# Optimization experiments

Measured on AMD Instinct MI355X. Metric: run time of the kernel, lower is better.

The kernel has to match this reference:

```python
import jax, jax.numpy as jnp
import numpy as np

H = 1024
NUM_HEADS = 16
E = 4
I = H * 4 // E  # expert intermediate size = 1024
EPS = 1e-6


def layer_norm(x, g, b):
    mu = jnp.mean(x, axis=-1, keepdims=True)
    var = jnp.mean(jnp.square(x - mu), axis=-1, keepdims=True)
    return (x - mu) * jax.lax.rsqrt(var + EPS) * g + b


def setup_inputs() -> dict:
    key = jax.random.key(0)
    ks = jax.random.split(key, 12)
    B, Nq, Nkv = 4, 1024, 2048
    inp = {
        "query": jax.random.normal(ks[0], (B, Nq, H), jnp.float32),
        "key_value": jax.random.normal(ks[1], (B, Nkv, H), jnp.float32),
        "Wq": jax.random.normal(ks[2], (H, H), jnp.float32) * 0.02,
        "bq": jnp.zeros((H,), jnp.float32),
        "Wk": jax.random.normal(ks[3], (H, H), jnp.float32) * 0.02,
        "bk": jnp.zeros((H,), jnp.float32),
        "Wv": jax.random.normal(ks[4], (H, H), jnp.float32) * 0.02,
        "bv": jnp.zeros((H,), jnp.float32),
        "Wo": jax.random.normal(ks[5], (H, H), jnp.float32) * 0.02,
        "bo": jnp.zeros((H,), jnp.float32),
        "g1": jnp.ones((H,), jnp.float32),
        "b1": jnp.zeros((H,), jnp.float32),
        "g2": jnp.ones((H,), jnp.float32),
        "b2": jnp.zeros((H,), jnp.float32),
        "gate_up": jax.random.normal(ks[6], (E, H, 2 * I), jnp.float32) * 0.02,
        "down": jax.random.normal(ks[7], (E, I, H), jnp.float32) * 0.02,
    }
    return inp


def reference(query, key_value, Wq, bq, Wk, bk, Wv, bv, Wo, bo,
              g1, b1, g2, b2, gate_up, down):
    B, Nq, _ = query.shape
    Nkv = key_value.shape[1]
    d = H // NUM_HEADS
    scale = d ** -0.5

    # ---- cross-attention with pre-norm + residual ----
    x = layer_norm(query, g1, b1)
    q = (x @ Wq + bq).reshape(B, Nq, NUM_HEADS, d)
    k = (key_value @ Wk + bk).reshape(B, Nkv, NUM_HEADS, d)
    v = (key_value @ Wv + bv).reshape(B, Nkv, NUM_HEADS, d)
    scores = jnp.einsum("bqhd,bkhd->bhqk", q, k) * scale
    attn = jax.nn.softmax(scores, axis=-1)
    ctx = jnp.einsum("bhqk,bkhd->bqhd", attn, v).reshape(B, Nq, H)
    x = query + (ctx @ Wo + bo)

    # ---- token-routed MoE SwiGLU MLP (expert = pos % E) ----
    residual = x
    h = layer_norm(x, g2, b2)
    outs = []
    for e in range(E):
        xe = h[:, e::E]                      # [B, Nq/E, H] tokens routed to expert e
        gu = xe @ gate_up[e]                 # [B, Nq/E, 2I]
        gate, up = gu[..., :I], gu[..., I:]
        inter = jax.nn.silu(gate) * up
        outs.append(inter @ down[e])         # [B, Nq/E, H]
    moe = jnp.stack(outs, axis=2).reshape(B, Nq, H)  # interleave back to position order
    return residual + moe
```

## Files before the change

### kernel.cpp

```cpp
#include <hip/hip_runtime.h>
#include <hip/hip_bf16.h>

typedef unsigned short u16;
typedef float f32x4 __attribute__((ext_vector_type(4)));
typedef short s16x8 __attribute__((ext_vector_type(8)));

__device__ __forceinline__ u16 f2b(float f) {
    union { float f; unsigned u; } c; c.f = f;
    unsigned r = c.u + 0x7fffu + ((c.u >> 16) & 1u);
    return (u16)(r >> 16);
}
__device__ __forceinline__ unsigned pkbf16(float a, float b) {
    union { __hip_bfloat162 h; unsigned u; } c;
    c.h = __float22bfloat162_rn(float2{a, b});
    return c.u;
}

#define ASYNC_COPY16(gp, lp)                                                       \
    __builtin_amdgcn_global_load_lds(                                              \
        (const __attribute__((address_space(1))) void*)(gp),                       \
        (__attribute__((address_space(3))) void*)(lp), 16, 0, 0)

__device__ __forceinline__ void transcast_body(const float* __restrict__ Wz,
                                               u16* __restrict__ Wtz,
                                               int K, int N, int bx, int by,
                                               int permute) {
    __shared__ float tile[64][65];
    const int n0 = bx * 64, k0 = by * 64;
    const int tid = threadIdx.x;
    const int tx = tid & 15, ty = tid >> 4;
#pragma unroll
    for (int it = 0; it < 4; it++) {
        int r = ty + it * 16;
        float4 v = *(const float4*)&Wz[(size_t)(k0 + r) * N + n0 + tx * 4];
        tile[r][tx * 4 + 0] = v.x;
        tile[r][tx * 4 + 1] = v.y;
        tile[r][tx * 4 + 2] = v.z;
        tile[r][tx * 4 + 3] = v.w;
    }
    __syncthreads();
    int n = tid >> 2;
    int ks = (tid & 3) * 16;
    int drow = n0 + n;
    if (permute) drow = (drow < 1024) ? 2 * drow : 2 * (drow - 1024) + 1;
    u16* dst = &Wtz[(size_t)drow * K + k0 + ks];
#pragma unroll
    for (int h = 0; h < 2; h++) {
        uint4 o;
        o.x = pkbf16(tile[ks + h * 8 + 0][n], tile[ks + h * 8 + 1][n]);
        o.y = pkbf16(tile[ks + h * 8 + 2][n], tile[ks + h * 8 + 3][n]);
        o.z = pkbf16(tile[ks + h * 8 + 4][n], tile[ks + h * 8 + 5][n]);
        o.w = pkbf16(tile[ks + h * 8 + 6][n], tile[ks + h * 8 + 7][n]);
        *(uint4*)(dst + h * 8) = o;
    }
}

__device__ __forceinline__ void cast_body(const float* __restrict__ x,
                                          u16* __restrict__ y, int blk) {
    int id = blk * 256 + threadIdx.x;
    const float* p = x + (size_t)id * 8;
    float4 a = *(const float4*)p;
    float4 b = *(const float4*)(p + 4);
    uint4 o;
    o.x = pkbf16(a.x, a.y);
    o.y = pkbf16(a.z, a.w);
    o.z = pkbf16(b.x, b.y);
    o.w = pkbf16(b.z, b.w);
    *(uint4*)(y + (size_t)id * 8) = o;
}

__device__ __forceinline__ void ln_body(const float* __restrict__ x,
                                        const float* __restrict__ g,
                                        const float* __restrict__ bb,
                                        u16* __restrict__ out, int token, int pack) {
    int tid = threadIdx.x;
    const float* row = x + (size_t)token * 1024;
    float4 v = *(const float4*)(row + tid * 4);
    float s1 = v.x + v.y + v.z + v.w;
    float s2 = v.x * v.x + v.y * v.y + v.z * v.z + v.w * v.w;
#pragma unroll
    for (int off = 32; off > 0; off >>= 1) {
        s1 += __shfl_down(s1, off);
        s2 += __shfl_down(s2, off);
    }
    __shared__ float ws1[4], ws2[4];
    int wave = tid >> 6;
    if ((tid & 63) == 0) { ws1[wave] = s1; ws2[wave] = s2; }
    __syncthreads();
    float t1 = ws1[0] + ws1[1] + ws1[2] + ws1[3];
    float t2 = ws2[0] + ws2[1] + ws2[2] + ws2[3];
    float mean = t1 * (1.f / 1024.f);
    float var = t2 * (1.f / 1024.f) - mean * mean;
    float rstd = rsqrtf(var + 1e-6f);
    size_t dest = token;
    if (pack) {
        int bq = token >> 10, q = token & 1023;
        dest = (size_t)(q & 3) * 1024 + (size_t)bq * 256 + (q >> 2);
    }
    int c = tid * 4;
    float4 gv = *(const float4*)(g + c);
    float4 bv = *(const float4*)(bb + c);
    uint2 o;
    o.x = pkbf16((v.x - mean) * rstd * gv.x + bv.x, (v.y - mean) * rstd * gv.y + bv.y);
    o.y = pkbf16((v.z - mean) * rstd * gv.z + bv.z, (v.w - mean) * rstd * gv.w + bv.w);
    *(uint2*)&out[dest * 1024 + c] = o;
}

__global__ __launch_bounds__(256) void ln_kernel(const float* __restrict__ x,
                                                 const float* __restrict__ g,
                                                 const float* __restrict__ bb,
                                                 u16* __restrict__ out, int pack) {
    ln_body(x, g, bb, out, blockIdx.x, pack);
}

__global__ __launch_bounds__(256) void prep_kernel(
    const float* __restrict__ Wq, const float* __restrict__ Wk,
    const float* __restrict__ Wv, const float* __restrict__ Wo,
    u16* __restrict__ wqt, u16* __restrict__ wkt,
    u16* __restrict__ wvt, u16* __restrict__ wot,
    const float* __restrict__ gate_up, u16* __restrict__ gut,
    const float* __restrict__ down, u16* __restrict__ dnt,
    const float* __restrict__ key_value, u16* __restrict__ kvbf,
    const float* __restrict__ query, const float* __restrict__ g1,
    const float* __restrict__ b1, u16* __restrict__ xn) {
    const int idx = blockIdx.x;
    if (idx < 1024) {
        int z = idx >> 8, r = idx & 255;
        const float* W = (z == 0) ? Wq : (z == 1) ? Wk : (z == 2) ? Wv : Wo;
        u16* O = (z == 0) ? wqt : (z == 1) ? wkt : (z == 2) ? wvt : wot;
        transcast_body(W, O, 1024, 1024, r >> 4, r & 15, 0);
    } else if (idx < 3072) {
        int t = idx - 1024, z = t >> 9, r = t & 511;
        transcast_body(gate_up + (size_t)z * 2097152, gut + (size_t)z * 2097152,
                       1024, 2048, r >> 4, r & 15, 1);
    } else if (idx < 4096) {
        int t = idx - 3072, z = t >> 8, r = t & 255;
        transcast_body(down + (size_t)z * 1048576, dnt + (size_t)z * 1048576,
                       1024, 1024, r >> 4, r & 15, 0);
    } else if (idx < 8192) {
        cast_body(key_value, kvbf, idx - 4096);
    } else {
        ln_body(query, g1, b1, xn, idx - 8192, 0);
    }
}

template <int BM>
__device__ __forceinline__ void gemm_body(
    u16* As, u16* Bs,
    const u16* __restrict__ Ab, const u16* __restrict__ Bb,
    const float* __restrict__ bias0, const float* __restrict__ bias1, int biasSplit,
    const float* __restrict__ resid,
    float* __restrict__ outF, u16* __restrict__ outH, u16* __restrict__ outH2,
    int N, int K, long long oStride, int z, int mode, float outScale,
    int m0, int n0) {
    constexpr int NJ = (BM == 128) ? 4 : 2;
    const int tid = threadIdx.x;
    const int wave = tid >> 6, lane = tid & 63;
    const int wm = (BM == 128) ? (wave >> 1) * 64 : 0;
    const int wn = (BM == 128) ? (wave & 1) * 64 : wave * 32;
    const int quad = lane >> 4, l16 = lane & 15;
    f32x4 acc[4][NJ] = {};
    for (int k0 = 0; k0 < K; k0 += 64) {
#pragma unroll
        for (int i = 0; i < BM / 32; i++) {
            int id = tid + i * 256;
            int row = id >> 3, c = id & 7;
            int srcseg = c ^ (row & 7);
            ASYNC_COPY16(&Ab[(size_t)(m0 + row) * K + k0 + srcseg * 8],
                         As + (size_t)(wave * 64 + i * 256) * 8);
        }
#pragma unroll
        for (int i = 0; i < 4; i++) {
            int id = tid + i * 256;
            int row = id >> 3, c = id & 7;
            int srcseg = c ^ (row & 7);
            ASYNC_COPY16(&Bb[(size_t)(n0 + row) * K + k0 + srcseg * 8],
                         Bs + (size_t)(wave * 64 + i * 256) * 8);
        }
        __syncthreads();
#pragma unroll
        for (int kk = 0; kk < 2; kk++) {
            s16x8 af[4], bfr[NJ];
#pragma unroll
            for (int i = 0; i < 4; i++) {
                int row = wm + i * 16 + l16;
                af[i] = *(const s16x8*)&As[row * 64 + ((kk * 4 + quad) ^ (row & 7)) * 8];
            }
#pragma unroll
            for (int j = 0; j < NJ; j++) {
                int row = wn + j * 16 + l16;
                bfr[j] = *(const s16x8*)&Bs[row * 64 + ((kk * 4 + quad) ^ (row & 7)) * 8];
            }
#pragma unroll
            for (int i = 0; i < 4; i++)
#pragma unroll
                for (int j = 0; j < NJ; j++)
                    acc[i][j] = __builtin_amdgcn_mfma_f32_16x16x32_bf16(af[i], bfr[j], acc[i][j], 0, 0, 0);
        }
        __syncthreads();
    }
#pragma unroll
    for (int i = 0; i < 4; i++) {
#pragma unroll
        for (int j = 0; j < NJ; j++) {
            int col = n0 + wn + j * 16 + l16;
            float bv = 0.f;
            if (bias0) bv = (col < biasSplit) ? bias0[col] : bias1[col - biasSplit];
            if (mode == 3) {
                float vr[4];
#pragma unroll
                for (int r = 0; r < 4; r++) vr[r] = acc[i][j][r] + bv;
                int row0 = m0 + wm + i * 16 + quad * 4;
                if (col < 1024) {
#pragma unroll
                    for (int r = 0; r < 4; r++)
                        outH[(size_t)(row0 + r) * 1024 + col] = f2b(vr[r]);
                } else {
                    int bb2 = row0 >> 11, key = row0 & 2047;
                    int hh = (col - 1024) >> 6, d = (col - 1024) & 63;
                    uint2 dw;
                    dw.x = pkbf16(vr[0], vr[1]);
                    dw.y = pkbf16(vr[2], vr[3]);
                    *(uint2*)&outH2[(((size_t)bb2 * 16 + hh) * 64 + d) * 2048 + key] = dw;
                }
                continue;
            }
#pragma unroll
            for (int r = 0; r < 4; r++) {
                int row = m0 + wm + i * 16 + quad * 4 + r;
                float v = acc[i][j][r] + bv;
                if (mode == 2) {
                    float other = __shfl_xor(v, 1);
                    if (!(lane & 1)) {
                        float res = (v / (1.f + __expf(-v))) * other;
                        outH[(size_t)z * oStride + (size_t)row * (N >> 1) + (col >> 1)] = f2b(res);
                    }
                } else if (mode == 1) {
                    int bb2 = row >> 8, qi = row & 255;
                    size_t oidx = ((size_t)bb2 * 1024 + (size_t)z + 4 * (size_t)qi) * N + col;
                    outF[oidx] = v + resid[oidx];
                } else {
                    size_t oidx = (size_t)z * oStride + (size_t)row * N + col;
                    if (resid) v += resid[oidx];
                    if (outF) outF[oidx] = v;
                    else outH[oidx] = f2b(v * outScale);
                }
            }
        }
    }
}

template <int BM>
__global__ __launch_bounds__(256) void gemm_t(
    const u16* __restrict__ A, const u16* __restrict__ Bt,
    const float* __restrict__ bias0, const float* __restrict__ bias1, int biasSplit,
    const float* __restrict__ resid,
    float* __restrict__ outF, u16* __restrict__ outH, u16* __restrict__ outH2,
    int N, int K,
    long long aStride, long long bStride, long long oStride,
    int mode, float outScale) {
    extern __shared__ __align__(16) u16 ldsb[];
    const int z = blockIdx.z;
    gemm_body<BM>(ldsb, ldsb + BM * 64,
                  A + (size_t)z * aStride, Bt + (size_t)z * bStride,
                  bias0, bias1, biasSplit, resid, outF, outH, outH2,
                  N, K, oStride, z, mode, outScale,
                  blockIdx.y * BM, blockIdx.x * 128);
}

__global__ __launch_bounds__(256) void gemm_qkv(
    const u16* __restrict__ xn, const u16* __restrict__ wqt,
    const float* __restrict__ bq,
    const u16* __restrict__ kvbf, const u16* __restrict__ kvw,
    const float* __restrict__ bk, const float* __restrict__ bv,
    u16* __restrict__ qb, u16* __restrict__ kvb, u16* __restrict__ vtb,
    float qscale) {
    extern __shared__ __align__(16) u16 ldsb[];
    const int bid = blockIdx.x;
    if (bid < 1024) {
        gemm_body<128>(ldsb, ldsb + 128 * 64, kvbf, kvw,
                       bk, bv, 1024, nullptr, nullptr, kvb, vtb,
                       2048, 1024, 0, 0, 3, 1.f,
                       (bid >> 4) * 128, (bid & 15) * 128);
    } else {
        int t = bid - 1024;
        gemm_body<64>(ldsb, ldsb + 64 * 64, xn, wqt,
                      bq, bq, 1 << 30, nullptr, nullptr, qb, nullptr,
                      1024, 1024, 0, 0, 0, qscale,
                      (t >> 3) * 64, (t & 7) * 128);
    }
}

__global__ __launch_bounds__(256) void flash_attn(
    const u16* __restrict__ Q, const u16* __restrict__ Kb,
    const u16* __restrict__ VT, u16* __restrict__ O) {
    const int lidx = blockIdx.x;
    const int xcd = lidx & 7, slot = lidx >> 3;
    const int g = xcd + 8 * (slot >> 4);
    const int qt = slot & 15;
    const int b = g >> 4, h = g & 15;
    const int tid = threadIdx.x, wave = tid >> 6, lane = tid & 63;
    const int quad = lane >> 4, l16 = lane & 15;
    const int q0 = qt * 64 + wave * 16;

    __shared__ __align__(16) u16 Ks[64 * 64];
    __shared__ __align__(16) u16 Vs[64 * 64];

    const size_t qrow = ((size_t)b * 1024 + q0 + l16) * 1024 + (size_t)h * 64;
    s16x8 qf0 = *(const s16x8*)&Q[qrow + quad * 8];
    s16x8 qf1 = *(const s16x8*)&Q[qrow + 32 + quad * 8];

    f32x4 o[4] = {};
    float l = 0.f;

    const u16* Kbh = Kb + ((size_t)b * 2048) * 1024 + (size_t)h * 64;
    const u16* VTbh = VT + (((size_t)b * 16 + h) * 64) * 2048;
    const uint4* Ks128 = (const uint4*)Ks;
    const uint4* Vs128 = (const uint4*)Vs;

    const int srow = tid >> 3, sc = tid & 7;
    const int ga = 4 * (sc >> 2) + 2 * (sc & 1);
    const int o8 = ((sc >> 1) & 1) * 8;

    for (int kc = 0; kc < 2048; kc += 64) {
        __syncthreads();
#pragma unroll
        for (int i = 0; i < 2; i++) {
            int id = tid + i * 256;
            int row = id >> 3;
            int srcseg = (id & 7) ^ (row & 7);
            ASYNC_COPY16(Kbh + (size_t)(kc + row) * 1024 + srcseg * 8,
                         &Ks[(size_t)(wave * 64 + i * 256) * 8]);
        }
#pragma unroll
        for (int i = 0; i < 2; i++) {
            int row = srow + i * 32;
            uint4 v = *(const uint4*)(VTbh + (size_t)row * 2048 + kc + sc * 8);
            char* rowp = (char*)&Vs[row * 64];
            *(uint2*)(rowp + ((ga ^ (row & 7)) * 16) + o8) = uint2{v.x, v.y};
            *(uint2*)(rowp + (((ga + 1) ^ (row & 7)) * 16) + o8) = uint2{v.z, v.w};
        }
        __syncthreads();

        f32x4 s[4];
#pragma unroll
        for (int kt = 0; kt < 4; kt++) {
            int row = kt * 16 + l16;
            union { uint4 v; s16x8 f; } a0, a1;
            a0.v = Ks128[row * 8 + (quad ^ (row & 7))];
            a1.v = Ks128[row * 8 + ((4 + quad) ^ (row & 7))];
            f32x4 acc = {};
            acc = __builtin_amdgcn_mfma_f32_16x16x32_bf16(a0.f, qf0, acc, 0, 0, 0);
            acc = __builtin_amdgcn_mfma_f32_16x16x32_bf16(a1.f, qf1, acc, 0, 0, 0);
            s[kt] = acc;
        }

        float p[16], rs = 0.f;
#pragma unroll
        for (int kt = 0; kt < 4; kt++)
#pragma unroll
            for (int r = 0; r < 4; r++) {
                float e = exp2f(s[kt][r]);
                p[kt * 4 + r] = e;
                rs += e;
            }
        rs += __shfl_xor(rs, 16);
        rs += __shfl_xor(rs, 32);
        l += rs;

        uint2 dw[4];
#pragma unroll
        for (int kt = 0; kt < 4; kt++) {
            dw[kt].x = pkbf16(p[kt * 4 + 0], p[kt * 4 + 1]);
            dw[kt].y = pkbf16(p[kt * 4 + 2], p[kt * 4 + 3]);
        }

#pragma unroll
        for (int c2 = 0; c2 < 2; c2++) {
            union { uint4 v; s16x8 f; } pf;
            pf.v = uint4{dw[2 * c2].x, dw[2 * c2].y, dw[2 * c2 + 1].x, dw[2 * c2 + 1].y};
#pragma unroll
            for (int dt = 0; dt < 4; dt++) {
                int row = dt * 16 + l16;
                union { uint4 v; s16x8 f; } vf;
                vf.v = Vs128[row * 8 + ((c2 * 4 + quad) ^ (row & 7))];
                o[dt] = __builtin_amdgcn_mfma_f32_16x16x32_bf16(vf.f, pf.f, o[dt], 0, 0, 0);
            }
        }
    }

    float inv = 1.f / l;
    size_t orow = ((size_t)b * 1024 + q0 + l16) * 1024 + (size_t)h * 64;
#pragma unroll
    for (int dt = 0; dt < 4; dt++) {
        uint2 dw;
        dw.x = pkbf16(o[dt][0] * inv, o[dt][1] * inv);
        dw.y = pkbf16(o[dt][2] * inv, o[dt][3] * inv);
        *(uint2*)&O[orow + dt * 16 + quad * 4] = dw;
    }
}

extern "C" void kernel_launch(void* const* d_in, const int* in_sizes, int n_in,
                              void* d_out, int out_size, void* d_ws, size_t ws_size,
                              hipStream_t stream) {
    (void)in_sizes; (void)n_in; (void)out_size; (void)ws_size;
    const float* query     = (const float*)d_in[0];
    const float* key_value = (const float*)d_in[1];
    const float* Wq = (const float*)d_in[2];
    const float* bq = (const float*)d_in[3];
    const float* Wk = (const float*)d_in[4];
    const float* bk = (const float*)d_in[5];
    const float* Wv = (const float*)d_in[6];
    const float* bv = (const float*)d_in[7];
    const float* Wo = (const float*)d_in[8];
    const float* bo = (const float*)d_in[9];
    const float* g1 = (const float*)d_in[10];
    const float* b1 = (const float*)d_in[11];
    const float* g2 = (const float*)d_in[12];
    const float* b2 = (const float*)d_in[13];
    const float* gate_up = (const float*)d_in[14];
    const float* down    = (const float*)d_in[15];
    float* out = (float*)d_out;

    char* wsb = (char*)d_ws;
    size_t off = 0;
    auto alloc = [&](size_t bytes) {
        char* p = wsb + off;
        off += (bytes + 255) & ~(size_t)255;
        return (void*)p;
    };
    u16* buf8a = (u16*)alloc((size_t)4096 * 1024 * 2);
    u16* qb    = (u16*)alloc((size_t)4096 * 1024 * 2);
    u16* kvb   = (u16*)alloc((size_t)8192 * 1024 * 2);
    u16* vtb   = (u16*)alloc((size_t)8192 * 1024 * 2);
    u16* kvbf  = (u16*)alloc((size_t)8192 * 1024 * 2);
    float* x2  = (float*)alloc((size_t)4096 * 1024 * 4);
    u16* wqt   = (u16*)alloc((size_t)1024 * 1024 * 2);
    u16* kvw   = (u16*)alloc((size_t)2048 * 1024 * 2);
    u16* wot   = (u16*)alloc((size_t)1024 * 1024 * 2);
    u16* gut   = (u16*)alloc((size_t)4 * 2048 * 1024 * 2);
    u16* dnt   = (u16*)alloc((size_t)4 * 1024 * 1024 * 2);
    u16* xn = buf8a; u16* ctx = buf8a; u16* hp = buf8a;
    u16* inter = kvbf;
    const int BIG = 1 << 30;
    const float QSCALE = 0.125f * 1.44269504f;

    prep_kernel<<<12288, 256, 0, stream>>>(
        Wq, Wk, Wv, Wo, wqt, kvw, kvw + (size_t)1024 * 1024, wot,
        gate_up, gut, down, dnt, key_value, kvbf, query, g1, b1, xn);
    gemm_qkv<<<1536, 256, 32768, stream>>>(xn, wqt, bq, kvbf, kvw, bk, bv,
                                           qb, kvb, vtb, QSCALE);
    flash_attn<<<1024, 256, 0, stream>>>(qb, kvb, vtb, ctx);
    gemm_t<64><<<dim3(8, 64, 1), 256, 24576, stream>>>(ctx, wot, bo, bo, BIG,
        query, x2, nullptr, nullptr, 1024, 1024, 0, 0, 0, 0, 1.f);
    ln_kernel<<<4096, 256, 0, stream>>>(x2, g2, b2, hp, 1);
    gemm_t<64><<<dim3(16, 16, 4), 256, 24576, stream>>>(hp, gut, nullptr, nullptr, BIG,
        nullptr, nullptr, inter, nullptr, 2048, 1024,
        (long long)1024 * 1024, (long long)2048 * 1024, (long long)1024 * 1024, 2, 1.f);
    gemm_t<64><<<dim3(8, 16, 4), 256, 24576, stream>>>(inter, dnt, nullptr, nullptr, BIG,
        x2, out, nullptr, nullptr, 1024, 1024,
        (long long)1024 * 1024, (long long)1024 * 1024, 0, 1, 1.f);
}
```

Measured before the change: 390.8 us.

## Double-buffer flash attention, pre-swizzle V tiles, process 32 queries per wave

The QKV GEMM now writes V^T in a per-64-key chunk layout that already carries the LDS swizzle, so flash attention can stage V with async global-to-LDS copies instead of register loads plus scattered LDS stores. K/V tiles are double-buffered, so the next chunk loads while the current one computes, leaving one barrier per iteration. Each wave now handles two 16-row query blocks, which reuses every K/V fragment read for twice the MFMAs, and the grid is halved. The row-sum shuffles are deferred to the end. The cost is more registers per thread and double the LDS per block, which may reduce occupancy.

New measurement: 392.7 us. Within noise of the previous version (+0.5%).

```diff
diff --git a/kernel.cpp b/kernel.cpp
--- a/kernel.cpp
+++ b/kernel.cpp
@@ -218,10 +218,15 @@
                 } else {
                     int bb2 = row0 >> 11, key = row0 & 2047;
                     int hh = (col - 1024) >> 6, d = (col - 1024) & 63;
+                    int cc = key >> 6, kk = key & 63;
+                    int kk4 = kk >> 4, q4 = (kk >> 2) & 3;
+                    int seg = (((kk4 >> 1) << 2) | q4) ^ (d & 7);
+                    int half = kk4 & 1;
                     uint2 dw;
                     dw.x = pkbf16(vr[0], vr[1]);
                     dw.y = pkbf16(vr[2], vr[3]);
-                    *(uint2*)&outH2[(((size_t)bb2 * 16 + hh) * 64 + d) * 2048 + key] = dw;
+                    *(uint2*)&outH2[((((size_t)bb2 * 16 + hh) * 32 + cc) * 64 + d) * 64
+                                    + seg * 8 + half * 4] = dw;
                 }
                 continue;
             }
@@ -296,107 +301,120 @@
     const u16* __restrict__ VT, u16* __restrict__ O) {
     const int lidx = blockIdx.x;
     const int xcd = lidx & 7, slot = lidx >> 3;
-    const int g = xcd + 8 * (slot >> 4);
-    const int qt = slot & 15;
+    const int g = xcd + 8 * (slot >> 3);
+    const int qt = slot & 7;
     const int b = g >> 4, h = g & 15;
     const int tid = threadIdx.x, wave = tid >> 6, lane = tid & 63;
     const int quad = lane >> 4, l16 = lane & 15;
-    const int q0 = qt * 64 + wave * 16;
-
-    __shared__ __align__(16) u16 Ks[64 * 64];
-    __shared__ __align__(16) u16 Vs[64 * 64];
-
-    const size_t qrow = ((size_t)b * 1024 + q0 + l16) * 1024 + (size_t)h * 64;
-    s16x8 qf0 = *(const s16x8*)&Q[qrow + quad * 8];
-    s16x8 qf1 = *(const s16x8*)&Q[qrow + 32 + quad * 8];
-
-    f32x4 o[4] = {};
-    float l = 0.f;
+    const int q0 = qt * 128 + wave * 32;
+
+    __shared__ __align__(16) u16 Ks[2][64 * 64];
+    __shared__ __align__(16) u16 Vs[2][64 * 64];
+
+    const size_t qrowA = ((size_t)b * 1024 + q0 + l16) * 1024 + (size_t)h * 64;
+    const size_t qrowB = qrowA + (size_t)16 * 1024;
+    s16x8 qA0 = *(const s16x8*)&Q[qrowA + quad * 8];
+    s16x8 qA1 = *(const s16x8*)&Q[qrowA + 32 + quad * 8];
+    s16x8 qB0 = *(const s16x8*)&Q[qrowB + quad * 8];
+    s16x8 qB1 = *(const s16x8*)&Q[qrowB + 32 + quad * 8];
+
+    f32x4 oA[4] = {}, oB[4] = {};
+    float lA = 0.f, lB = 0.f;
 
     const u16* Kbh = Kb + ((size_t)b * 2048) * 1024 + (size_t)h * 64;
-    const u16* VTbh = VT + (((size_t)b * 16 + h) * 64) * 2048;
-    const uint4* Ks128 = (const uint4*)Ks;
-    const uint4* Vs128 = (const uint4*)Vs;
-
-    const int srow = tid >> 3, sc = tid & 7;
-    const int ga = 4 * (sc >> 2) + 2 * (sc & 1);
-    const int o8 = ((sc >> 1) & 1) * 8;
-
-    for (int kc = 0; kc < 2048; kc += 64) {
-        __syncthreads();
+    const u16* Vbh = VT + ((size_t)(b * 16 + h) * 32) * 4096;
+
+    auto stage = [&](int c, int buf) {
+        const int kc = c * 64;
+        u16* Kd = &Ks[buf][0];
+        u16* Vd = &Vs[buf][0];
 #pragma unroll
         for (int i = 0; i < 2; i++) {
             int id = tid + i * 256;
             int row = id >> 3;
             int srcseg = (id & 7) ^ (row & 7);
             ASYNC_COPY16(Kbh + (size_t)(kc + row) * 1024 + srcseg * 8,
-                         &Ks[(size_t)(wave * 64 + i * 256) * 8]);
-        }
+                         Kd + (size_t)(wave * 64 + i * 256) * 8);
+        }
+        const u16* Vc = Vbh + (size_t)c * 4096;
 #pragma unroll
         for (int i = 0; i < 2; i++) {
-            int row = srow + i * 32;
-            uint4 v = *(const uint4*)(VTbh + (size_t)row * 2048 + kc + sc * 8);
-            char* rowp = (char*)&Vs[row * 64];
-            *(uint2*)(rowp + ((ga ^ (row & 7)) * 16) + o8) = uint2{v.x, v.y};
-            *(uint2*)(rowp + (((ga + 1) ^ (row & 7)) * 16) + o8) = uint2{v.z, v.w};
-        }
+            ASYNC_COPY16(Vc + (size_t)(tid + i * 256) * 8,
+                         Vd + (size_t)(wave * 64 + i * 256) * 8);
+        }
+    };
+
+    stage(0, 0);
+    for (int c = 0; c < 32; c++) {
         __syncthreads();
-
-        f32x4 s[4];
+        if (c < 31) stage(c + 1, (c + 1) & 1);
+        const uint4* Kp = (const uint4*)&Ks[c & 1][0];
+        const uint4* Vp = (const uint4*)&Vs[c & 1][0];
+
+        f32x4 sA[4], sB[4];
 #pragma unroll
         for (int kt = 0; kt < 4; kt++) {
             int row = kt * 16 + l16;
             union { uint4 v; s16x8 f; } a0, a1;
-            a0.v = Ks128[row * 8 + (quad ^ (row & 7))];
-            a1.v = Ks128[row * 8 + ((4 + quad) ^ (row & 7))];
+            a0.v = Kp[row * 8 + (quad ^ (row & 7))];
+            a1.v = Kp[row * 8 + ((4 + quad) ^ (row & 7))];
             f32x4 acc = {};
-            acc = __builtin_amdgcn_mfma_f32_16x16x32_bf16(a0.f, qf0, acc, 0, 0, 0);
-            acc = __builtin_amdgcn_mfma_f32_16x16x32_bf16(a1.f, qf1, acc, 0, 0, 0);
-            s[kt] = acc;
-        }
-
-        float p[16], rs = 0.f;
-#pragma unroll
-        for (int kt = 0; kt < 4; kt++)
-#pragma unroll
-            for (int r = 0; r < 4; r++) {
-                float e = exp2f(s[kt][r]);
-                p[kt * 4 + r] = e;
-                rs += e;
-            }
-        rs += __shfl_xor(rs, 16);
-        rs += __shfl_xor(rs, 32);
-        l += rs;
-
-        uint2 dw[4];
+            acc = __builtin_amdgcn_mfma_f32_16x16x32_bf16(a0.f, qA0, acc, 0, 0, 0);
+            sA[kt] = __builtin_amdgcn_mfma_f32_16x16x32_bf16(a1.f, qA1, acc, 0, 0, 0);
+            f32x4 accB = {};
+            accB = __builtin_amdgcn_mfma_f32_16x16x32_bf16(a0.f, qB0, accB, 0, 0, 0);
+            sB[kt] = __builtin_amdgcn_mfma_f32_16x16x32_bf16(a1.f, qB1, accB, 0, 0, 0);
+        }
+
+        uint2 dwA[4], dwB[4];
+        float rsA = 0.f, rsB = 0.f;
 #pragma unroll
         for (int kt = 0; kt < 4; kt++) {
-            dw[kt].x = pkbf16(p[kt * 4 + 0], p[kt * 4 + 1]);
-            dw[kt].y = pkbf16(p[kt * 4 + 2], p[kt * 4 + 3]);
-        }
+            float p0 = exp2f(sA[kt][0]), p1 = exp2f(sA[kt][1]);
+            float p2 = exp2f(sA[kt][2]), p3 = exp2f(sA[kt][3]);
+            rsA += (p0 + p1) + (p2 + p3);
+            dwA[kt].x = pkbf16(p0, p1);
+            dwA[kt].y = pkbf16(p2, p3);
+        }
+        lA += rsA;
+#pragma unroll
+        for (int kt = 0; kt < 4; kt++) {
+            float p0 = exp2f(sB[kt][0]), p1 = exp2f(sB[kt][1]);
+            float p2 = exp2f(sB[kt][2]), p3 = exp2f(sB[kt][3]);
+            rsB += (p0 + p1) + (p2 + p3);
+            dwB[kt].x = pkbf16(p0, p1);
+            dwB[kt].y = pkbf16(p2, p3);
+        }
+        lB += rsB;
 
 #pragma unroll
         for (int c2 = 0; c2 < 2; c2++) {
-            union { uint4 v; s16x8 f; } pf;
-            pf.v = uint4{dw[2 * c2].x, dw[2 * c2].y, dw[2 * c2 + 1].x, dw[2 * c2 + 1].y};
+            union { uint4 v; s16x8 f; } pfA, pfB;
+            pfA.v = uint4{dwA[2 * c2].x, dwA[2 * c2].y, dwA[2 * c2 + 1].x, dwA[2 * c2 + 1].y};
+            pfB.v = uint4{dwB[2 * c2].x, dwB[2 * c2].y, dwB[2 * c2 + 1].x, dwB[2 * c2 + 1].y};
 #pragma unroll
             for (int dt = 0; dt < 4; dt++) {
                 int row = dt * 16 + l16;
                 union { uint4 v; s16x8 f; } vf;
-                vf.v = Vs128[row * 8 + ((c2 * 4 + quad) ^ (row & 7))];
-                o[dt] = __builtin_amdgcn_mfma_f32_16x16x32_bf16(vf.f, pf.f, o[dt], 0, 0, 0);
+                vf.v = Vp[row * 8 + ((c2 * 4 + quad) ^ (row & 7))];
+                oA[dt] = __builtin_amdgcn_mfma_f32_16x16x32_bf16(vf.f, pfA.f, oA[dt], 0, 0, 0);
+                oB[dt] = __builtin_amdgcn_mfma_f32_16x16x32_bf16(vf.f, pfB.f, oB[dt], 0, 0, 0);
             }
         }
     }
 
-    float inv = 1.f / l;
-    size_t orow = ((size_t)b * 1024 + q0 + l16) * 1024 + (size_t)h * 64;
+    lA += __shfl_xor(lA, 16); lA += __shfl_xor(lA, 32);
+    lB += __shfl_xor(lB, 16); lB += __shfl_xor(lB, 32);
+    float invA = 1.f / lA, invB = 1.f / lB;
 #pragma unroll
     for (int dt = 0; dt < 4; dt++) {
         uint2 dw;
-        dw.x = pkbf16(o[dt][0] * inv, o[dt][1] * inv);
-        dw.y = pkbf16(o[dt][2] * inv, o[dt][3] * inv);
-        *(uint2*)&O[orow + dt * 16 + quad * 4] = dw;
+        dw.x = pkbf16(oA[dt][0] * invA, oA[dt][1] * invA);
+        dw.y = pkbf16(oA[dt][2] * invA, oA[dt][3] * invA);
+        *(uint2*)&O[qrowA + dt * 16 + quad * 4] = dw;
+        dw.x = pkbf16(oB[dt][0] * invB, oB[dt][1] * invB);
+        dw.y = pkbf16(oB[dt][2] * invB, oB[dt][3] * invB);
+        *(uint2*)&O[qrowB + dt * 16 + quad * 4] = dw;
     }
 }
 
@@ -450,7 +468,7 @@
         gate_up, gut, down, dnt, key_value, kvbf, query, g1, b1, xn);
     gemm_qkv<<<1536, 256, 32768, stream>>>(xn, wqt, bq, kvbf, kvw, bk, bv,
                                            qb, kvb, vtb, QSCALE);
-    flash_attn<<<1024, 256, 0, stream>>>(qb, kvb, vtb, ctx);
+    flash_attn<<<512, 256, 0, stream>>>(qb, kvb, vtb, ctx);
     gemm_t<64><<<dim3(8, 64, 1), 256, 24576, stream>>>(ctx, wot, bo, bo, BIG,
         query, x2, nullptr, nullptr, 1024, 1024, 0, 0, 0, 0, 1.f);
     ln_kernel<<<4096, 256, 0, stream>>>(x2, g2, b2, hp, 1);
```

## Pre-tile V layout, double-buffer flash attention, enlarge GEMM tiles

Applied to the files above, without the earlier changes.

The QKV GEMM epilogue now writes V transposed into per-64-key chunk tiles already swizzled to match the attention kernel's LDS layout. This lets flash attention load V with async global-to-LDS copies instead of register round-trips. Flash attention moves to 512-thread blocks covering 128 queries, double-buffers K and V so the next chunk loads while the current one computes, and defers the row-sum shuffle reduction to the end. All projection and MoE GEMMs switch from 64-row to 128-row tiles, reducing block counts at the cost of more LDS per block and possibly lower occupancy.

Result: slower. 430.2 us (+10.1%).

```diff
diff --git a/kernel.cpp b/kernel.cpp
--- a/kernel.cpp
+++ b/kernel.cpp
@@ -218,10 +218,15 @@
                 } else {
                     int bb2 = row0 >> 11, key = row0 & 2047;
                     int hh = (col - 1024) >> 6, d = (col - 1024) & 63;
+                    int cc = key >> 6, kk = key & 63;
+                    int kk4 = kk >> 4, q4 = (kk >> 2) & 3;
+                    int seg = (((kk4 >> 1) << 2) | q4) ^ (d & 7);
+                    int half = kk4 & 1;
                     uint2 dw;
                     dw.x = pkbf16(vr[0], vr[1]);
                     dw.y = pkbf16(vr[2], vr[3]);
-                    *(uint2*)&outH2[(((size_t)bb2 * 16 + hh) * 64 + d) * 2048 + key] = dw;
+                    *(uint2*)&outH2[((((size_t)bb2 * 16 + hh) * 32 + cc) * 64 + d) * 64
+                                    + seg * 8 + half * 4] = dw;
                 }
                 continue;
             }
@@ -284,27 +289,27 @@
                        (bid >> 4) * 128, (bid & 15) * 128);
     } else {
         int t = bid - 1024;
-        gemm_body<64>(ldsb, ldsb + 64 * 64, xn, wqt,
-                      bq, bq, 1 << 30, nullptr, nullptr, qb, nullptr,
-                      1024, 1024, 0, 0, 0, qscale,
-                      (t >> 3) * 64, (t & 7) * 128);
-    }
-}
-
-__global__ __launch_bounds__(256) void flash_attn(
+        gemm_body<128>(ldsb, ldsb + 128 * 64, xn, wqt,
+                       bq, bq, 1 << 30, nullptr, nullptr, qb, nullptr,
+                       1024, 1024, 0, 0, 0, qscale,
+                       (t >> 3) * 128, (t & 7) * 128);
+    }
+}
+
+__global__ __launch_bounds__(512) void flash_attn(
     const u16* __restrict__ Q, const u16* __restrict__ Kb,
     const u16* __restrict__ VT, u16* __restrict__ O) {
     const int lidx = blockIdx.x;
     const int xcd = lidx & 7, slot = lidx >> 3;
-    const int g = xcd + 8 * (slot >> 4);
-    const int qt = slot & 15;
+    const int g = xcd + 8 * (slot >> 3);
+    const int qt = slot & 7;
     const int b = g >> 4, h = g & 15;
     const int tid = threadIdx.x, wave = tid >> 6, lane = tid & 63;
     const int quad = lane >> 4, l16 = lane & 15;
-    const int q0 = qt * 64 + wave * 16;
-
-    __shared__ __align__(16) u16 Ks[64 * 64];
-    __shared__ __align__(16) u16 Vs[64 * 64];
+    const int q0 = qt * 128 + wave * 16;
+
+    __shared__ __align__(16) u16 Ks[2][64 * 64];
+    __shared__ __align__(16) u16 Vs[2][64 * 64];
 
     const size_t qrow = ((size_t)b * 1024 + q0 + l16) * 1024 + (size_t)h * 64;
     s16x8 qf0 = *(const s16x8*)&Q[qrow + quad * 8];
@@ -314,66 +319,48 @@
     float l = 0.f;
 
     const u16* Kbh = Kb + ((size_t)b * 2048) * 1024 + (size_t)h * 64;
-    const u16* VTbh = VT + (((size_t)b * 16 + h) * 64) * 2048;
-    const uint4* Ks128 = (const uint4*)Ks;
-    const uint4* Vs128 = (const uint4*)Vs;
-
-    const int srow = tid >> 3, sc = tid & 7;
-    const int ga = 4 * (sc >> 2) + 2 * (sc & 1);
-    const int o8 = ((sc >> 1) & 1) * 8;
-
-    for (int kc = 0; kc < 2048; kc += 64) {
+    const u16* Vbh = VT + ((size_t)(b * 16 + h) * 32) * 4096;
+
+    const int krow = tid >> 3;
+    const int ksrcseg = (tid & 7) ^ (krow & 7);
+
+    auto stage = [&](int c, int buf) {
+        ASYNC_COPY16(Kbh + (size_t)(c * 64 + krow) * 1024 + ksrcseg * 8,
+                     &Ks[buf][(size_t)(wave * 64) * 8]);
+        ASYNC_COPY16(Vbh + (size_t)c * 4096 + (size_t)tid * 8,
+                     &Vs[buf][(size_t)(wave * 64) * 8]);
+    };
+
+    stage(0, 0);
+    for (int c = 0; c < 32; c++) {
         __syncthreads();
-#pragma unroll
-        for (int i = 0; i < 2; i++) {
-            int id = tid + i * 256;
-            int row = id >> 3;
-            int srcseg = (id & 7) ^ (row & 7);
-            ASYNC_COPY16(Kbh + (size_t)(kc + row) * 1024 + srcseg * 8,
-                         &Ks[(size_t)(wave * 64 + i * 256) * 8]);
-        }
-#pragma unroll
-        for (int i = 0; i < 2; i++) {
-            int row = srow + i * 32;
-            uint4 v = *(const uint4*)(VTbh + (size_t)row * 2048 + kc + sc * 8);
-            char* rowp = (char*)&Vs[row * 64];
-            *(uint2*)(rowp + ((ga ^ (row & 7)) * 16) + o8) = uint2{v.x, v.y};
-            *(uint2*)(rowp + (((ga + 1) ^ (row & 7)) * 16) + o8) = uint2{v.z, v.w};
-        }
-        __syncthreads();
+        if (c < 31) stage(c + 1, (c + 1) & 1);
+        const uint4* Kp = (const uint4*)&Ks[c & 1][0];
+        const uint4* Vp = (const uint4*)&Vs[c & 1][0];
 
         f32x4 s[4];
 #pragma unroll
         for (int kt = 0; kt < 4; kt++) {
             int row = kt * 16 + l16;
             union { uint4 v; s16x8 f; } a0, a1;
-            a0.v = Ks128[row * 8 + (quad ^ (row & 7))];
-            a1.v = Ks128[row * 8 + ((4 + quad) ^ (row & 7))];
+            a0.v = Kp[row * 8 + (quad ^ (row & 7))];
+            a1.v = Kp[row * 8 + ((4 + quad) ^ (row & 7))];
             f32x4 acc = {};
             acc = __builtin_amdgcn_mfma_f32_16x16x32_bf16(a0.f, qf0, acc, 0, 0, 0);
-            acc = __builtin_amdgcn_mfma_f32_16x16x32_bf16(a1.f, qf1, acc, 0, 0, 0);
-            s[kt] = acc;
-        }
-
-        float p[16], rs = 0.f;
-#pragma unroll
-        for (int kt = 0; kt < 4; kt++)
-#pragma unroll
-            for (int r = 0; r < 4; r++) {
-                float e = exp2f(s[kt][r]);
-                p[kt * 4 + r] = e;
-                rs += e;
-            }
-        rs += __shfl_xor(rs, 16);
-        rs += __shfl_xor(rs, 32);
+            s[kt] = __builtin_amdgcn_mfma_f32_16x16x32_bf16(a1.f, qf1, acc, 0, 0, 0);
+        }
+
+        uint2 dw[4];
+        float rs = 0.f;
+#pragma unroll
+        for (int kt = 0; kt < 4; kt++) {
+            float p0 = exp2f(s[kt][0]), p1 = exp2f(s[kt][1]);
+            float p2 = exp2f(s[kt][2]), p3 = exp2f(s[kt][3]);
+            rs += (p0 + p1) + (p2 + p3);
+            dw[kt].x = pkbf16(p0, p1);
+            dw[kt].y = pkbf16(p2, p3);
+        }
         l += rs;
-
-        uint2 dw[4];
-#pragma unroll
-        for (int kt = 0; kt < 4; kt++) {
-            dw[kt].x = pkbf16(p[kt * 4 + 0], p[kt * 4 + 1]);
-            dw[kt].y = pkbf16(p[kt * 4 + 2], p[kt * 4 + 3]);
-        }
 
 #pragma unroll
         for (int c2 = 0; c2 < 2; c2++) {
@@ -383,20 +370,21 @@
             for (int dt = 0; dt < 4; dt++) {
                 int row = dt * 16 + l16;
                 union { uint4 v; s16x8 f; } vf;
-                vf.v = Vs128[row * 8 + ((c2 * 4 + quad) ^ (row & 7))];
+                vf.v = Vp[row * 8 + ((c2 * 4 + quad) ^ (row & 7))];
                 o[dt] = __builtin_amdgcn_mfma_f32_16x16x32_bf16(vf.f, pf.f, o[dt], 0, 0, 0);
             }
         }
     }
 
+    l += __shfl_xor(l, 16);
+    l += __shfl_xor(l, 32);
     float inv = 1.f / l;
-    size_t orow = ((size_t)b * 1024 + q0 + l16) * 1024 + (size_t)h * 64;
 #pragma unroll
     for (int dt = 0; dt < 4; dt++) {
         uint2 dw;
         dw.x = pkbf16(o[dt][0] * inv, o[dt][1] * inv);
         dw.y = pkbf16(o[dt][2] * inv, o[dt][3] * inv);
-        *(uint2*)&O[orow + dt * 16 + quad * 4] = dw;
+        *(uint2*)&O[qrow + dt * 16 + quad * 4] = dw;
     }
 }
 
@@ -448,16 +436,16 @@
     prep_kernel<<<12288, 256, 0, stream>>>(
         Wq, Wk, Wv, Wo, wqt, kvw, kvw + (size_t)1024 * 1024, wot,
         gate_up, gut, down, dnt, key_value, kvbf, query, g1, b1, xn);
-    gemm_qkv<<<1536, 256, 32768, stream>>>(xn, wqt, bq, kvbf, kvw, bk, bv,
+    gemm_qkv<<<1280, 256, 32768, stream>>>(xn, wqt, bq, kvbf, kvw, bk, bv,
                                            qb, kvb, vtb, QSCALE);
-    flash_attn<<<1024, 256, 0, stream>>>(qb, kvb, vtb, ctx);
-    gemm_t<64><<<dim3(8, 64, 1), 256, 24576, stream>>>(ctx, wot, bo, bo, BIG,
+    flash_attn<<<512, 512, 0, stream>>>(qb, kvb, vtb, ctx);
+    gemm_t<128><<<dim3(8, 32, 1), 256, 32768, stream>>>(ctx, wot, bo, bo, BIG,
         query, x2, nullptr, nullptr, 1024, 1024, 0, 0, 0, 0, 1.f);
     ln_kernel<<<4096, 256, 0, stream>>>(x2, g2, b2, hp, 1);
-    gemm_t<64><<<dim3(16, 16, 4), 256, 24576, stream>>>(hp, gut, nullptr, nullptr, BIG,
+    gemm_t<128><<<dim3(16, 8, 4), 256, 32768, stream>>>(hp, gut, nullptr, nullptr, BIG,
         nullptr, nullptr, inter, nullptr, 2048, 1024,
         (long long)1024 * 1024, (long long)2048 * 1024, (long long)1024 * 1024, 2, 1.f);
-    gemm_t<64><<<dim3(8, 16, 4), 256, 24576, stream>>>(inter, dnt, nullptr, nullptr, BIG,
+    gemm_t<128><<<dim3(8, 8, 4), 256, 32768, stream>>>(inter, dnt, nullptr, nullptr, BIG,
         x2, out, nullptr, nullptr, 1024, 1024,
         (long long)1024 * 1024, (long long)1024 * 1024, 0, 1, 1.f);
 }
```
